# Kernel optimization log

Hardware: AMD Instinct MI355X
Metric: run time of the kernel (lower is better)

Reference implementation:

```python
import jax, jax.numpy as jnp
import numpy as np

B, T, C, H = 4, 2048, 1024, 16
D = C // H


def setup_inputs() -> dict:
    key = jax.random.key(0)
    ks = jax.random.split(key, 5)
    s = C ** -0.5  # keep linear outputs O(1) like standard init
    x = jax.random.normal(ks[0], (B, T, C), dtype=jnp.float32)
    Wq = jax.random.normal(ks[1], (C, C), dtype=jnp.float32) * s
    Wk = jax.random.normal(ks[2], (C, C), dtype=jnp.float32) * s
    Wv = jax.random.normal(ks[3], (C, C), dtype=jnp.float32) * s
    Wproj = jax.random.normal(ks[4], (C, C), dtype=jnp.float32) * s
    alpha_raw = jnp.zeros((1, H, 1, 1), dtype=jnp.float32)
    beta_raw = jnp.zeros((1, H, 1, 1), dtype=jnp.float32)
    state = jnp.zeros((B, H, D, D), dtype=jnp.float32)
    return dict(x=x, Wq=Wq, Wk=Wk, Wv=Wv, Wproj=Wproj,
                alpha_raw=alpha_raw, beta_raw=beta_raw, state=state)


def reference(x, Wq, Wk, Wv, Wproj, alpha_raw, beta_raw, state):
    Bx, Tx, Cx = x.shape
    Hn = alpha_raw.shape[1]
    Dh = Cx // Hn
    # projections (torch Linear: x @ W^T), split heads -> (B, H, T, D)
    def proj(W):
        return (x @ W.T).reshape(Bx, Tx, Hn, Dh).transpose(0, 2, 1, 3)
    q, k, v = proj(Wq), proj(Wk), proj(Wv)
    # F.normalize(k, dim=-1) with eps=1e-12
    k = k / jnp.maximum(jnp.linalg.norm(k, axis=-1, keepdims=True), 1e-12)
    alpha = jax.nn.sigmoid(alpha_raw) * 0.5  # (1, H, 1, 1)
    beta = jax.nn.sigmoid(beta_raw) * 0.5

    def step(st, qkv):
        qt, kt, vt = qkv  # each (B, H, D)
        # y_t = q_t @ state^T
        y = jnp.einsum('bhe,bhde->bhd', qt, st)
        # Mk = state @ k_t
        Mk = jnp.einsum('bhde,bhe->bhd', st, kt)
        st = st - alpha * jnp.einsum('bhd,bhe->bhde', Mk, kt) \
                + beta * jnp.einsum('bhd,bhe->bhde', vt, kt)
        return st, y

    # scan over time: (T, B, H, D)
    qT = q.transpose(2, 0, 1, 3)
    kT = k.transpose(2, 0, 1, 3)
    vT = v.transpose(2, 0, 1, 3)
    state_f, ys = jax.lax.scan(step, state, (qT, kT, vT))
    y = ys.transpose(1, 0, 2, 3).reshape(Bx, Tx, Cx)  # (B, T, C)
    out = y @ Wproj.T
    return out, state_f
```

## Files before the change

kernel.cpp:

```cpp
#include <hip/hip_runtime.h>
#include <hip/hip_bf16.h>
#include <cstdint>

#define B_ 4
#define T_ 2048
#define C_ 1024
#define H_ 16
#define D_ 64
#define NC_ 32
#define L_ 64

typedef __attribute__((ext_vector_type(8))) short bf16x8;
typedef __attribute__((ext_vector_type(4))) float f32x4;

static __device__ __forceinline__ unsigned short f2bf(float f) {
  unsigned u = __float_as_uint(f);
  u += 0x7fff + ((u >> 16) & 1);
  return (unsigned short)(u >> 16);
}
static __device__ __forceinline__ float bf2f(unsigned short b) {
  return __uint_as_float(((unsigned)b) << 16);
}
static __device__ __forceinline__ int swz128(int row, int byte) {
  return row * 128 + (byte ^ ((row & 7) << 4));
}

#define LDS_BARRIER() asm volatile("s_waitcnt lgkmcnt(0)\ns_barrier" ::: "memory")

__global__ __launch_bounds__(256) void cvt_all(const float* __restrict__ x,
                                               const float* __restrict__ wq,
                                               const float* __restrict__ wk,
                                               const float* __restrict__ wv,
                                               const float* __restrict__ wp,
                                               unsigned short* __restrict__ xbf,
                                               unsigned short* __restrict__ W3,
                                               unsigned short* __restrict__ Wp) {
  const int bidx = blockIdx.x;
  const float* src;
  unsigned short* dst;
  long base;
  if (bidx < 8192) {
    src = x; dst = xbf; base = (long)bidx * 1024;
  } else {
    const int g = (bidx - 8192) >> 10;
    src = (g == 0) ? wq : (g == 1) ? wk : (g == 2) ? wv : wp;
    dst = (g < 3) ? (W3 + (long)g * 1048576) : Wp;
    base = (long)((bidx - 8192) & 1023) * 1024;
  }
  long i = base + threadIdx.x * 4;
  float4 v = *reinterpret_cast<const float4*>(src + i);
  ushort4 o;
  o.x = f2bf(v.x); o.y = f2bf(v.y); o.z = f2bf(v.z); o.w = f2bf(v.w);
  *reinterpret_cast<ushort4*>(dst + i) = o;
}


#define STAGEH(GP, GR0, KT, LOFF) do {                                            \
    const unsigned short* _s = (GP) + ((GR0) + wid * 8 + lr8) * 1024L             \
                               + (long)(KT) * 64 + skb * 8;                       \
    char* _d = (char*)lds + (LOFF) + wid * 1024;                                  \
    __builtin_amdgcn_global_load_lds((const __attribute__((address_space(1))) void*)_s,      \
        (__attribute__((address_space(3))) void*)_d, 16, 0, 0);                   \
    __builtin_amdgcn_global_load_lds((const __attribute__((address_space(1))) void*)(_s + 64 * 1024L), \
        (__attribute__((address_space(3))) void*)(_d + 8192), 16, 0, 0);          \
  } while (0)

#define READF(AV, BV, RG) do {                                                    \
    const char* ab_ = (const char*)lds + (RG) + arow;                             \
    const char* bb_ = (const char*)lds + (RG) + 16384 + brow;                     \
    _Pragma("unroll")                                                             \
    for (int j = 0; j < 4; ++j) {                                                 \
      AV[j][0] = *(const bf16x8*)(ab_ + j * 4096 + cb0);                          \
      AV[j][1] = *(const bf16x8*)(ab_ + j * 4096 + cb1);                          \
    }                                                                             \
    _Pragma("unroll")                                                             \
    for (int n = 0; n < 4; ++n) {                                                 \
      BV[n][0] = *(const bf16x8*)(bb_ + n * 8192 + cb0);                          \
      BV[n][1] = *(const bf16x8*)(bb_ + n * 8192 + cb1);                          \
    }                                                                             \
  } while (0)

#define MFMA32(AV, BV) do {                                                       \
    _Pragma("unroll")                                                             \
    for (int j = 0; j < 4; ++j)                                                   \
      _Pragma("unroll")                                                           \
      for (int n = 0; n < 4; ++n)                                                 \
        acc[j][n] = __builtin_amdgcn_mfma_f32_16x16x32_bf16(                      \
            AV[j][0], BV[n][0], acc[j][n], 0, 0, 0);                              \
    _Pragma("unroll")                                                             \
    for (int j = 0; j < 4; ++j)                                                   \
      _Pragma("unroll")                                                           \
      for (int n = 0; n < 4; ++n)                                                 \
        acc[j][n] = __builtin_amdgcn_mfma_f32_16x16x32_bf16(                      \
            AV[j][1], BV[n][1], acc[j][n], 0, 0, 0);                              \
  } while (0)

#define PIPHASE(T, CA, CB, NA, NB) do {                                           \
    READF(NA, NB, (((T) + 1) % 3) * 49152);                                       \
    {                                                                             \
      const int ts_ = ((T) + 3 > 15) ? 15 : (T) + 3;                              \
      const int sg_ = ((T) % 3) * 49152;                                          \
      STAGEH(Bw, bN, ts_, sg_ + 16384);                                           \
      STAGEH(Bw, bN + 128, ts_, sg_ + 32768);                                     \
      STAGEH(A, bM, ts_, sg_);                                                    \
    }                                                                             \
    __builtin_amdgcn_s_setprio(1);                                                \
    MFMA32(CA, CB);                                                               \
    __builtin_amdgcn_s_setprio(0);                                                \
    asm volatile("s_waitcnt lgkmcnt(0)" ::: "memory");                            \
    asm volatile("s_waitcnt vmcnt(6)" ::: "memory");                              \
    __builtin_amdgcn_s_barrier();                                                 \
  } while (0)

template<int OUT_BF16>
__global__ __launch_bounds__(512, 2) void gemm128x256(
    const unsigned short* __restrict__ A,
    const unsigned short* __restrict__ Bw,
    void* __restrict__ Cp, int N) {
  __shared__ __align__(16) char lds[147456];
  const int tid = threadIdx.x;
  const int wid = tid >> 6, lane = tid & 63;
  const int wm = wid >> 2, wn = wid & 3;
  const int f = lane & 15, g = lane >> 4;
  const int lr8 = lane >> 3, lc = lane & 7;
  const int skb = lc ^ lr8;
  const int bid = blockIdx.y * gridDim.x + blockIdx.x;
  const int cpx = (gridDim.x * gridDim.y) >> 3;
  const int sw = (bid & 7) * cpx + (bid >> 3);
  const long bM = (long)(sw / gridDim.x) * 128;
  const long bN = (long)(sw % gridDim.x) * 256;
  const int cb0 = ((0 + g) ^ (f & 7)) * 16;
  const int cb1 = ((4 + g) ^ (f & 7)) * 16;
  const int arow = (wm * 16 + f) * 128;
  const int brow = (wn * 16 + f) * 128;

  f32x4 acc[4][4] = {};
  bf16x8 avA[4][2], bvA[4][2], avB[4][2], bvB[4][2];

  STAGEH(Bw, bN, 0, 16384);
  STAGEH(Bw, bN + 128, 0, 32768);
  STAGEH(A, bM, 0, 0);
  STAGEH(Bw, bN, 1, 49152 + 16384);
  STAGEH(Bw, bN + 128, 1, 49152 + 32768);
  STAGEH(A, bM, 1, 49152);
  STAGEH(Bw, bN, 2, 98304 + 16384);
  STAGEH(Bw, bN + 128, 2, 98304 + 32768);
  STAGEH(A, bM, 2, 98304);
  asm volatile("s_waitcnt vmcnt(6)" ::: "memory");
  __builtin_amdgcn_s_barrier();
  READF(avA, bvA, 0);
  asm volatile("s_waitcnt lgkmcnt(0)" ::: "memory");
  __builtin_amdgcn_s_barrier();

#pragma unroll
  for (int i = 0; i < 8; ++i) {
    PIPHASE(2 * i,     avA, bvA, avB, bvB);
    PIPHASE(2 * i + 1, avB, bvB, avA, bvA);
  }
  asm volatile("s_waitcnt vmcnt(0)" ::: "memory");

#pragma unroll
  for (int mf = 0; mf < 4; ++mf) {
    long row = bM + mf * 32 + wm * 16 + g * 4;
#pragma unroll
    for (int nf = 0; nf < 4; ++nf) {
      long col = bN + (nf >> 1) * 128 + (nf & 1) * 64 + wn * 16 + f;
#pragma unroll
      for (int r = 0; r < 4; ++r) {
        if (OUT_BF16)
          ((unsigned short*)Cp)[(row + r) * (long)N + col] = f2bf(acc[mf][nf][r]);
        else
          ((float*)Cp)[(row + r) * (long)N + col] = acc[mf][nf][r];
      }
    }
  }
}

__global__ __launch_bounds__(256) void chunk_prep(
    unsigned short* __restrict__ qkv,
    const float* __restrict__ a_raw, const float* __restrict__ b_raw,
    unsigned short* __restrict__ Ubuf, unsigned short* __restrict__ Wbuf,
    unsigned short* __restrict__ SLbuf) {
  __shared__ __align__(16) unsigned short sK[64 * 64];
  __shared__ __align__(16) unsigned short sQ[64 * 64];
  __shared__ __align__(16) unsigned short sV[64 * 64];
  __shared__ float sA[64 * 64];

  const int blk = blockIdx.x;
  const int bh = blk >> 5, c = blk & 31;
  const int b = bh >> 4, h = bh & 15;
  const int tid = threadIdx.x;
  const int wid = tid >> 6, lane = tid & 63;

  const float alpha = 0.5f / (1.f + __expf(-a_raw[h]));
  const float beta  = 0.5f / (1.f + __expf(-b_raw[h]));

  {
    const int row = tid >> 2, cg = tid & 3;
    unsigned short* gp = qkv + (long)(b * 2048 + c * 64 + row) * 3072 + h * 64 + cg * 16;
    bf16x8 q0 = *(const bf16x8*)(gp);
    bf16x8 q1 = *(const bf16x8*)(gp + 8);
    bf16x8 k0 = *(const bf16x8*)(gp + 1024);
    bf16x8 k1 = *(const bf16x8*)(gp + 1024 + 8);
    bf16x8 v0 = *(const bf16x8*)(gp + 2048);
    bf16x8 v1 = *(const bf16x8*)(gp + 2048 + 8);
    float kf[16];
    float ss = 0.f;
#pragma unroll
    for (int i = 0; i < 8; ++i) { kf[i] = bf2f((unsigned short)k0[i]); ss += kf[i] * kf[i]; }
#pragma unroll
    for (int i = 0; i < 8; ++i) { kf[8 + i] = bf2f((unsigned short)k1[i]); ss += kf[8 + i] * kf[8 + i]; }
    ss += __shfl_xor(ss, 1);
    ss += __shfl_xor(ss, 2);
    const float inv = 1.f / fmaxf(sqrtf(ss), 1e-12f);
    bf16x8 n0, n1;
#pragma unroll
    for (int i = 0; i < 8; ++i) { n0[i] = (short)f2bf(kf[i] * inv); n1[i] = (short)f2bf(kf[8 + i] * inv); }
    *(bf16x8*)((char*)sK + swz128(row, cg * 32)) = n0;
    *(bf16x8*)((char*)sK + swz128(row, cg * 32 + 16)) = n1;
    *(bf16x8*)((char*)sQ + swz128(row, cg * 32)) = q0;
    *(bf16x8*)((char*)sQ + swz128(row, cg * 32 + 16)) = q1;
    *(bf16x8*)((char*)sV + row * 128 + cg * 32) = v0;
    *(bf16x8*)((char*)sV + row * 128 + cg * 32 + 16) = v1;
  }
  __syncthreads();

  {
    const int erow = tid >> 2, tq = tid & 3;
    unsigned short kt[16];
#pragma unroll
    for (int i = 0; i < 16; ++i)
      kt[i] = *(const unsigned short*)((const char*)sK + swz128(tq * 16 + i, 2 * erow));
    unsigned short* vp = qkv + (long)(b * 2048 + c * 64 + erow) * 3072 + 2048 + h * 64 + tq * 16;
    *(bf16x8*)vp = *(const bf16x8*)kt;
    *(bf16x8*)(vp + 8) = *(const bf16x8*)(kt + 8);
  }

  const int rfrag = lane & 15, koff = (lane >> 4) * 8, crow = (lane >> 4) * 4;
  const int w2 = wid & 1;
  if (wid < 2) {
#pragma unroll
    for (int mt = 0; mt < 2; ++mt) {
      const int m = w2 * 2 + mt;
      const int ra = 16 * m + rfrag;
      f32x4 acc[4] = {};
#pragma unroll
      for (int ks = 0; ks < 2; ++ks) {
        bf16x8 af = *(const bf16x8*)((const char*)sK + swz128(ra, ks * 64 + koff * 2));
#pragma unroll
        for (int n = 0; n < 4; ++n) {
          bf16x8 bf = *(const bf16x8*)((const char*)sK + swz128(16 * n + rfrag, ks * 64 + koff * 2));
          acc[n] = __builtin_amdgcn_mfma_f32_16x16x32_bf16(af, bf, acc[n], 0, 0, 0);
        }
      }
#pragma unroll
      for (int n = 0; n < 4; ++n)
#pragma unroll
        for (int r = 0; r < 4; ++r)
          sA[(16 * m + crow + r) * 64 + 16 * n + rfrag] = acc[n][r];
    }
  } else {
#pragma unroll
    for (int mt = 0; mt < 2; ++mt) {
      const int m = w2 * 2 + mt;
      const int ra = 16 * m + rfrag;
      f32x4 acc[4] = {};
#pragma unroll
      for (int ks = 0; ks < 2; ++ks) {
        bf16x8 af = *(const bf16x8*)((const char*)sQ + swz128(ra, ks * 64 + koff * 2));
#pragma unroll
        for (int n = 0; n < 4; ++n) {
          bf16x8 bf = *(const bf16x8*)((const char*)sK + swz128(16 * n + rfrag, ks * 64 + koff * 2));
          acc[n] = __builtin_amdgcn_mfma_f32_16x16x32_bf16(af, bf, acc[n], 0, 0, 0);
        }
      }
#pragma unroll
      for (int n = 0; n < 4; ++n)
#pragma unroll
        for (int r = 0; r < 4; ++r) {
          int t = 16 * m + crow + r, j = 16 * n + rfrag;
          SLbuf[(long)blk * 4096 + t * 64 + j] = (j < t) ? f2bf(acc[n][r]) : (unsigned short)0;
        }
    }
  }
  __syncthreads();

  if (wid < 2) {
    const int d = lane;
    float x[64];
#pragma unroll
    for (int t = 0; t < 64; ++t) {
      float rhs;
      if (wid == 0) rhs = beta * bf2f(sV[t * 64 + d]);
      else          rhs = alpha * bf2f(*(const unsigned short*)((const char*)sK + swz128(t, 2 * d)));
      float s = 0.f;
#pragma unroll
      for (int j = 0; j < t; ++j) s = fmaf(sA[t * 64 + j], x[j], s);
      x[t] = rhs - alpha * s;
    }
    unsigned short* ob = (wid == 0 ? Ubuf : Wbuf) + (long)blk * 4096 + d;
#pragma unroll
    for (int t = 0; t < 64; ++t) ob[t * 64] = f2bf(x[t]);
  }
}

__global__ __launch_bounds__(256) void chunk_scan(
    const unsigned short* __restrict__ qkv,
    const unsigned short* __restrict__ Ubuf, const unsigned short* __restrict__ Wbuf,
    const unsigned short* __restrict__ SLbuf,
    const float* __restrict__ state_in, unsigned short* __restrict__ ybuf,
    float* __restrict__ state_out) {
  __shared__ __align__(16) char lds[73728];

  const int bid0 = blockIdx.x;
  const int blk = (bid0 & 7) * 32 + (bid0 >> 3);
  const int bh = blk >> 2, dq = blk & 3;
  const int b = bh >> 4, h = bh & 15;
  const int tid = threadIdx.x, wid = tid >> 6, lane = tid & 63;
  const int rfrag = lane & 15, koff = (lane >> 4) * 8, crow = (lane >> 4) * 4;
  const int row = tid >> 2, cg = tid & 3;

  char* gt = lds + 69632;
  char* ssb = lds + 71680;

  const unsigned short* gpb = qkv + (long)(b * 2048 + row) * 3072 + h * 64 + cg * 16;
  const long tbb = ((long)(bh * 32) * 64 + row) * 64 + cg * 16;
  const long ubb = ((long)(bh * 32) * 64 + (tid >> 1)) * 64 + dq * 16 + (tid & 1) * 8;

  bf16x8 qv0, qv1, kt0, kt1, wv0, wv1, sl0, sl1, uv;
#define LOADREGS(CN) do {                                                       \
    const unsigned short* gp = gpb + (long)(CN) * 64 * 3072;                    \
    const long tb = tbb + (long)(CN) * 4096;                                    \
    qv0 = *(const bf16x8*)gp;            qv1 = *(const bf16x8*)(gp + 8);        \
    kt0 = *(const bf16x8*)(gp + 2048);   kt1 = *(const bf16x8*)(gp + 2048 + 8); \
    wv0 = *(const bf16x8*)(Wbuf + tb);   wv1 = *(const bf16x8*)(Wbuf + tb + 8); \
    sl0 = *(const bf16x8*)(SLbuf + tb);  sl1 = *(const bf16x8*)(SLbuf + tb + 8);\
    if (tid < 128) uv = *(const bf16x8*)(Ubuf + ubb + (long)(CN) * 4096);       \
  } while (0)

#define WRITE_TILES(BUF) do {                                                   \
    char* bp_ = lds + (BUF) * 34816;                                            \
    *(bf16x8*)(bp_ + swz128(row, cg * 32)) = qv0;                               \
    *(bf16x8*)(bp_ + swz128(row, cg * 32 + 16)) = qv1;                          \
    *(bf16x8*)(bp_ + 8192 + swz128(row, cg * 32)) = wv0;                        \
    *(bf16x8*)(bp_ + 8192 + swz128(row, cg * 32 + 16)) = wv1;                   \
    *(bf16x8*)(bp_ + 16384 + swz128(row, cg * 32)) = sl0;                       \
    *(bf16x8*)(bp_ + 16384 + swz128(row, cg * 32 + 16)) = sl1;                  \
    *(bf16x8*)(bp_ + 24576 + swz128(row, cg * 32)) = kt0;                       \
    *(bf16x8*)(bp_ + 24576 + swz128(row, cg * 32 + 16)) = kt1;                  \
    if (tid < 128) *(bf16x8*)(bp_ + 32768 + ((tid >> 1) * 16 + (tid & 1) * 8) * 2) = uv; \
  } while (0)

  f32x4 sacc;
#pragma unroll
  for (int r = 0; r < 4; ++r)
    sacc[r] = state_in[(long)bh * 4096 + (dq * 16 + crow + r) * 64 + 16 * wid + rfrag];
#pragma unroll
  for (int r = 0; r < 4; ++r)
    *(unsigned short*)(ssb + swz128(crow + r, 2 * (16 * wid + rfrag))) = f2bf(sacc[r]);

  LOADREGS(0);
  WRITE_TILES(0);
  LOADREGS(1);
  LDS_BARRIER();

  for (int c = 0; c < NC_; ++c) {
    const int cur = c & 1;
    const char* bp = lds + cur * 34816;
    const int ta = 16 * wid + rfrag;

    f32x4 p = {};
    f32x4 yac = {};
#pragma unroll
    for (int ks = 0; ks < 2; ++ks) {
      bf16x8 afw = *(const bf16x8*)(bp + 8192 + swz128(ta, ks * 64 + koff * 2));
      bf16x8 afq = *(const bf16x8*)(bp + swz128(ta, ks * 64 + koff * 2));
      bf16x8 bS = *(const bf16x8*)(ssb + swz128(rfrag, ks * 64 + koff * 2));
      p = __builtin_amdgcn_mfma_f32_16x16x32_bf16(afw, bS, p, 0, 0, 0);
      yac = __builtin_amdgcn_mfma_f32_16x16x32_bf16(afq, bS, yac, 0, 0, 0);
    }
#pragma unroll
    for (int r = 0; r < 4; ++r) {
      int t = 16 * wid + crow + r;
      float gg = bf2f(*(const unsigned short*)(bp + 32768 + (t * 16 + rfrag) * 2)) - p[r];
      *(unsigned short*)(gt + swz128(rfrag, 2 * t)) = f2bf(gg);
    }
    LDS_BARRIER();

#pragma unroll
    for (int ks = 0; ks < 2; ++ks) {
      bf16x8 aSL = *(const bf16x8*)(bp + 16384 + swz128(ta, ks * 64 + koff * 2));
      bf16x8 bGT = *(const bf16x8*)(gt + swz128(rfrag, ks * 64 + koff * 2));
      yac = __builtin_amdgcn_mfma_f32_16x16x32_bf16(aSL, bGT, yac, 0, 0, 0);
    }
#pragma unroll
    for (int ks = 0; ks < 2; ++ks) {
      bf16x8 aGT = *(const bf16x8*)(gt + swz128(rfrag, ks * 64 + koff * 2));
      bf16x8 bKT = *(const bf16x8*)(bp + 24576 + swz128(16 * wid + rfrag, ks * 64 + koff * 2));
      sacc = __builtin_amdgcn_mfma_f32_16x16x32_bf16(aGT, bKT, sacc, 0, 0, 0);
    }
#pragma unroll
    for (int r = 0; r < 4; ++r) {
      int t = 16 * wid + crow + r;
      ybuf[(long)(b * 2048 + c * 64 + t) * 1024 + h * 64 + dq * 16 + rfrag] = f2bf(yac[r]);
    }
#pragma unroll
    for (int r = 0; r < 4; ++r)
      *(unsigned short*)(ssb + swz128(crow + r, 2 * (16 * wid + rfrag))) = f2bf(sacc[r]);
    if (c + 1 < NC_) {
      WRITE_TILES(cur ^ 1);
      int cn = c + 2; if (cn > NC_ - 1) cn = NC_ - 1;
      LOADREGS(cn);
    }
    LDS_BARRIER();
  }

#pragma unroll
  for (int r = 0; r < 4; ++r)
    state_out[(long)bh * 4096 + (dq * 16 + crow + r) * 64 + 16 * wid + rfrag] = sacc[r];
#undef LOADREGS
#undef WRITE_TILES
}

extern "C" void kernel_launch(void* const* d_in, const int* in_sizes, int n_in,
                              void* d_out, int out_size, void* d_ws, size_t ws_size,
                              hipStream_t stream) {
  (void)in_sizes; (void)n_in; (void)out_size; (void)ws_size;
  const float* x     = (const float*)d_in[0];
  const float* Wq    = (const float*)d_in[1];
  const float* Wk    = (const float*)d_in[2];
  const float* Wv    = (const float*)d_in[3];
  const float* Wproj = (const float*)d_in[4];
  const float* a_raw = (const float*)d_in[5];
  const float* b_raw = (const float*)d_in[6];
  const float* state = (const float*)d_in[7];

  char* ws = (char*)d_ws;
  unsigned short* xbf = (unsigned short*)ws;
  unsigned short* W3  = (unsigned short*)(ws + (16l << 20));
  unsigned short* Wp  = (unsigned short*)(ws + (22l << 20));
  unsigned short* qkv = (unsigned short*)(ws + (24l << 20));
  unsigned short* Ub  = (unsigned short*)(ws + (72l << 20));
  unsigned short* Wb  = (unsigned short*)(ws + (88l << 20));
  unsigned short* SLb = (unsigned short*)(ws + (104l << 20));
  float* out = (float*)d_out;
  float* state_out = out + (long)B_ * T_ * C_;

  cvt_all<<<dim3(12288), dim3(256), 0, stream>>>(x, Wq, Wk, Wv, Wproj, xbf, W3, Wp);

  gemm128x256<1><<<dim3(3072 / 256, 8192 / 128), dim3(512), 0, stream>>>(xbf, W3, (void*)qkv, 3072);

  chunk_prep<<<dim3(2048), dim3(256), 0, stream>>>(qkv, a_raw, b_raw, Ub, Wb, SLb);
  chunk_scan<<<dim3(256), dim3(256), 0, stream>>>(qkv, Ub, Wb, SLb, state, xbf, state_out);

  gemm128x256<0><<<dim3(1024 / 256, 8192 / 128), dim3(512), 0, stream>>>(xbf, Wp, (void*)out, 1024);
}
```

Before: 174.2 us.

## Load chunk-scan MFMA fragments directly from global into registers, drop LDS staging

The chunk scan kernel no longer stages the Q, K, W, SL and U tiles through double-buffered shared memory. Each lane now loads its MFMA fragments straight from global memory into ping-pong register sets, prefetching the next chunk while computing the current one. This shrinks LDS from 72KB to 4KB and removes the tile store/load round trip, which should allow more resident blocks. The U producer now writes U transposed so that each lane's fragment is contiguous. The cost is more register pressure and less coalesced global loads.

```diff
diff --git a/kernel.cpp b/kernel.cpp
--- a/kernel.cpp
+++ b/kernel.cpp
@@ -11,6 +11,7 @@
 #define L_ 64
 
 typedef __attribute__((ext_vector_type(8))) short bf16x8;
+typedef __attribute__((ext_vector_type(4))) short bf16x4;
 typedef __attribute__((ext_vector_type(4))) float f32x4;
 
 static __device__ __forceinline__ unsigned short f2bf(float f) {
@@ -53,7 +54,6 @@
   o.x = f2bf(v.x); o.y = f2bf(v.y); o.z = f2bf(v.z); o.w = f2bf(v.w);
   *reinterpret_cast<ushort4*>(dst + i) = o;
 }
-
 
 #define STAGEH(GP, GR0, KT, LOFF) do {                                            \
     const unsigned short* _s = (GP) + ((GR0) + wid * 8 + lr8) * 1024L             \
@@ -298,9 +298,18 @@
       for (int j = 0; j < t; ++j) s = fmaf(sA[t * 64 + j], x[j], s);
       x[t] = rhs - alpha * s;
     }
-    unsigned short* ob = (wid == 0 ? Ubuf : Wbuf) + (long)blk * 4096 + d;
-#pragma unroll
-    for (int t = 0; t < 64; ++t) ob[t * 64] = f2bf(x[t]);
+    if (wid == 0) {
+      unsigned short xb[64];
+#pragma unroll
+      for (int t = 0; t < 64; ++t) xb[t] = f2bf(x[t]);
+      unsigned short* ob = Ubuf + (long)blk * 4096 + (long)d * 64;
+#pragma unroll
+      for (int i = 0; i < 8; ++i) *(bf16x8*)(ob + i * 8) = *(const bf16x8*)(xb + i * 8);
+    } else {
+      unsigned short* ob = Wbuf + (long)blk * 4096 + d;
+#pragma unroll
+      for (int t = 0; t < 64; ++t) ob[t * 64] = f2bf(x[t]);
+    }
   }
 }
 
@@ -310,7 +319,7 @@
     const unsigned short* __restrict__ SLbuf,
     const float* __restrict__ state_in, unsigned short* __restrict__ ybuf,
     float* __restrict__ state_out) {
-  __shared__ __align__(16) char lds[73728];
+  __shared__ __align__(16) char lds[4096];
 
   const int bid0 = blockIdx.x;
   const int blk = (bid0 & 7) * 32 + (bid0 >> 3);
@@ -318,37 +327,62 @@
   const int b = bh >> 4, h = bh & 15;
   const int tid = threadIdx.x, wid = tid >> 6, lane = tid & 63;
   const int rfrag = lane & 15, koff = (lane >> 4) * 8, crow = (lane >> 4) * 4;
-  const int row = tid >> 2, cg = tid & 3;
-
-  char* gt = lds + 69632;
-  char* ssb = lds + 71680;
-
-  const unsigned short* gpb = qkv + (long)(b * 2048 + row) * 3072 + h * 64 + cg * 16;
-  const long tbb = ((long)(bh * 32) * 64 + row) * 64 + cg * 16;
-  const long ubb = ((long)(bh * 32) * 64 + (tid >> 1)) * 64 + dq * 16 + (tid & 1) * 8;
-
-  bf16x8 qv0, qv1, kt0, kt1, wv0, wv1, sl0, sl1, uv;
-#define LOADREGS(CN) do {                                                       \
-    const unsigned short* gp = gpb + (long)(CN) * 64 * 3072;                    \
-    const long tb = tbb + (long)(CN) * 4096;                                    \
-    qv0 = *(const bf16x8*)gp;            qv1 = *(const bf16x8*)(gp + 8);        \
-    kt0 = *(const bf16x8*)(gp + 2048);   kt1 = *(const bf16x8*)(gp + 2048 + 8); \
-    wv0 = *(const bf16x8*)(Wbuf + tb);   wv1 = *(const bf16x8*)(Wbuf + tb + 8); \
-    sl0 = *(const bf16x8*)(SLbuf + tb);  sl1 = *(const bf16x8*)(SLbuf + tb + 8);\
-    if (tid < 128) uv = *(const bf16x8*)(Ubuf + ubb + (long)(CN) * 4096);       \
-  } while (0)
-
-#define WRITE_TILES(BUF) do {                                                   \
-    char* bp_ = lds + (BUF) * 34816;                                            \
-    *(bf16x8*)(bp_ + swz128(row, cg * 32)) = qv0;                               \
-    *(bf16x8*)(bp_ + swz128(row, cg * 32 + 16)) = qv1;                          \
-    *(bf16x8*)(bp_ + 8192 + swz128(row, cg * 32)) = wv0;                        \
-    *(bf16x8*)(bp_ + 8192 + swz128(row, cg * 32 + 16)) = wv1;                   \
-    *(bf16x8*)(bp_ + 16384 + swz128(row, cg * 32)) = sl0;                       \
-    *(bf16x8*)(bp_ + 16384 + swz128(row, cg * 32 + 16)) = sl1;                  \
-    *(bf16x8*)(bp_ + 24576 + swz128(row, cg * 32)) = kt0;                       \
-    *(bf16x8*)(bp_ + 24576 + swz128(row, cg * 32 + 16)) = kt1;                  \
-    if (tid < 128) *(bf16x8*)(bp_ + 32768 + ((tid >> 1) * 16 + (tid & 1) * 8) * 2) = uv; \
+  const int ta = 16 * wid + rfrag;
+
+  char* gt  = lds;
+  char* ssb = lds + 2048;
+
+  const unsigned short* qbase  = qkv + (long)(b * 2048 + ta) * 3072 + h * 64 + koff;
+  const unsigned short* ktbase = qkv + (long)(b * 2048 + ta) * 3072 + 2048 + h * 64 + koff;
+  const unsigned short* wbase  = Wbuf + ((long)(bh * 32) * 64 + ta) * 64 + koff;
+  const unsigned short* slbase = SLbuf + ((long)(bh * 32) * 64 + ta) * 64 + koff;
+  const unsigned short* ubase  = Ubuf + (long)(bh * 32) * 4096 + (dq * 16 + rfrag) * 64 + 16 * wid + crow;
+
+#define LOADF(WS, QS, SS, KS, US, CN) do {                                      \
+    const long qo = (long)(CN) * 64 * 3072;                                     \
+    const long to = (long)(CN) * 4096;                                          \
+    WS[0] = *(const bf16x8*)(wbase + to);                                       \
+    WS[1] = *(const bf16x8*)(wbase + to + 32);                                  \
+    QS[0] = *(const bf16x8*)(qbase + qo);                                       \
+    QS[1] = *(const bf16x8*)(qbase + qo + 32);                                  \
+    SS[0] = *(const bf16x8*)(slbase + to);                                      \
+    SS[1] = *(const bf16x8*)(slbase + to + 32);                                 \
+    KS[0] = *(const bf16x8*)(ktbase + qo);                                      \
+    KS[1] = *(const bf16x8*)(ktbase + qo + 32);                                 \
+    US = *(const bf16x4*)(ubase + to);                                          \
+  } while (0)
+
+#define CHUNK_BODY(WC, QC, SC, KC, UC, WN, QN, SN, KN, UN, C) do {              \
+    if ((C) + 1 < NC_) LOADF(WN, QN, SN, KN, UN, (C) + 1);                      \
+                           \
+    bf16x8 bS0 = *(const bf16x8*)(ssb + swz128(rfrag, koff * 2));               \
+    bf16x8 bS1 = *(const bf16x8*)(ssb + swz128(rfrag, 64 + koff * 2));          \
+    f32x4 p = {}, yac = {};                                                     \
+    p   = __builtin_amdgcn_mfma_f32_16x16x32_bf16(WC[0], bS0, p, 0, 0, 0);      \
+    yac = __builtin_amdgcn_mfma_f32_16x16x32_bf16(QC[0], bS0, yac, 0, 0, 0);    \
+    p   = __builtin_amdgcn_mfma_f32_16x16x32_bf16(WC[1], bS1, p, 0, 0, 0);      \
+    yac = __builtin_amdgcn_mfma_f32_16x16x32_bf16(QC[1], bS1, yac, 0, 0, 0);    \
+    _Pragma("unroll")                                                           \
+    for (int r = 0; r < 4; ++r) {                                               \
+      int t = 16 * wid + crow + r;                                              \
+      float gg = bf2f((unsigned short)UC[r]) - p[r];                            \
+      *(unsigned short*)(gt + swz128(rfrag, 2 * t)) = f2bf(gg);                 \
+    }                                                                           \
+    LDS_BARRIER();                             \
+                                            \
+    bf16x8 g0 = *(const bf16x8*)(gt + swz128(rfrag, koff * 2));                 \
+    bf16x8 g1 = *(const bf16x8*)(gt + swz128(rfrag, 64 + koff * 2));            \
+    yac  = __builtin_amdgcn_mfma_f32_16x16x32_bf16(SC[0], g0, yac, 0, 0, 0);    \
+    sacc = __builtin_amdgcn_mfma_f32_16x16x32_bf16(g0, KC[0], sacc, 0, 0, 0);   \
+    yac  = __builtin_amdgcn_mfma_f32_16x16x32_bf16(SC[1], g1, yac, 0, 0, 0);    \
+    sacc = __builtin_amdgcn_mfma_f32_16x16x32_bf16(g1, KC[1], sacc, 0, 0, 0);   \
+    _Pragma("unroll")                                                           \
+    for (int r = 0; r < 4; ++r) {                                               \
+      int t = 16 * wid + crow + r;                                              \
+      ybuf[(long)(b * 2048 + (C) * 64 + t) * 1024 + h * 64 + dq * 16 + rfrag] = f2bf(yac[r]); \
+      *(unsigned short*)(ssb + swz128(crow + r, 2 * (16 * wid + rfrag))) = f2bf(sacc[r]); \
+    }                                                                           \
+    LDS_BARRIER();         \
   } while (0)
 
   f32x4 sacc;
@@ -359,67 +393,21 @@
   for (int r = 0; r < 4; ++r)
     *(unsigned short*)(ssb + swz128(crow + r, 2 * (16 * wid + rfrag))) = f2bf(sacc[r]);
 
-  LOADREGS(0);
-  WRITE_TILES(0);
-  LOADREGS(1);
+  bf16x8 wA[2], qA[2], slA[2], kA[2]; bf16x4 uA;
+  bf16x8 wB[2], qB[2], slB[2], kB[2]; bf16x4 uB;
+  LOADF(wA, qA, slA, kA, uA, 0);
   LDS_BARRIER();
 
-  for (int c = 0; c < NC_; ++c) {
-    const int cur = c & 1;
-    const char* bp = lds + cur * 34816;
-    const int ta = 16 * wid + rfrag;
-
-    f32x4 p = {};
-    f32x4 yac = {};
-#pragma unroll
-    for (int ks = 0; ks < 2; ++ks) {
-      bf16x8 afw = *(const bf16x8*)(bp + 8192 + swz128(ta, ks * 64 + koff * 2));
-      bf16x8 afq = *(const bf16x8*)(bp + swz128(ta, ks * 64 + koff * 2));
-      bf16x8 bS = *(const bf16x8*)(ssb + swz128(rfrag, ks * 64 + koff * 2));
-      p = __builtin_amdgcn_mfma_f32_16x16x32_bf16(afw, bS, p, 0, 0, 0);
-      yac = __builtin_amdgcn_mfma_f32_16x16x32_bf16(afq, bS, yac, 0, 0, 0);
-    }
-#pragma unroll
-    for (int r = 0; r < 4; ++r) {
-      int t = 16 * wid + crow + r;
-      float gg = bf2f(*(const unsigned short*)(bp + 32768 + (t * 16 + rfrag) * 2)) - p[r];
-      *(unsigned short*)(gt + swz128(rfrag, 2 * t)) = f2bf(gg);
-    }
-    LDS_BARRIER();
-
-#pragma unroll
-    for (int ks = 0; ks < 2; ++ks) {
-      bf16x8 aSL = *(const bf16x8*)(bp + 16384 + swz128(ta, ks * 64 + koff * 2));
-      bf16x8 bGT = *(const bf16x8*)(gt + swz128(rfrag, ks * 64 + koff * 2));
-      yac = __builtin_amdgcn_mfma_f32_16x16x32_bf16(aSL, bGT, yac, 0, 0, 0);
-    }
-#pragma unroll
-    for (int ks = 0; ks < 2; ++ks) {
-      bf16x8 aGT = *(const bf16x8*)(gt + swz128(rfrag, ks * 64 + koff * 2));
-      bf16x8 bKT = *(const bf16x8*)(bp + 24576 + swz128(16 * wid + rfrag, ks * 64 + koff * 2));
-      sacc = __builtin_amdgcn_mfma_f32_16x16x32_bf16(aGT, bKT, sacc, 0, 0, 0);
-    }
-#pragma unroll
-    for (int r = 0; r < 4; ++r) {
-      int t = 16 * wid + crow + r;
-      ybuf[(long)(b * 2048 + c * 64 + t) * 1024 + h * 64 + dq * 16 + rfrag] = f2bf(yac[r]);
-    }
-#pragma unroll
-    for (int r = 0; r < 4; ++r)
-      *(unsigned short*)(ssb + swz128(crow + r, 2 * (16 * wid + rfrag))) = f2bf(sacc[r]);
-    if (c + 1 < NC_) {
-      WRITE_TILES(cur ^ 1);
-      int cn = c + 2; if (cn > NC_ - 1) cn = NC_ - 1;
-      LOADREGS(cn);
-    }
-    LDS_BARRIER();
+  for (int c = 0; c < NC_; c += 2) {
+    CHUNK_BODY(wA, qA, slA, kA, uA, wB, qB, slB, kB, uB, c);
+    CHUNK_BODY(wB, qB, slB, kB, uB, wA, qA, slA, kA, uA, c + 1);
   }
 
 #pragma unroll
   for (int r = 0; r < 4; ++r)
     state_out[(long)bh * 4096 + (dq * 16 + crow + r) * 64 + 16 * wid + rfrag] = sacc[r];
-#undef LOADREGS
-#undef WRITE_TILES
+#undef LOADF
+#undef CHUNK_BODY
 }
 
 extern "C" void kernel_launch(void* const* d_in, const int* in_sizes, int n_in,
```

Result: slower. 182.3 us (+4.6%).
